# Performance work log

Hardware: AMD Instinct MI355X
Metric: run time of the kernel (lower is better)

Reference implementation:

```python
import jax, jax.numpy as jnp
import numpy as np

N = 50000      # num_nodes
E = 500000     # num_edges
D_IN = 128     # in_features
D_OUT = 128    # out_features
D_REL = 128    # nrela_dim
NEG_SLOPE = 0.2   # LeakyReLU alpha
RATIO = 0.5       # float ratio -> simple (non-schedule) branch
LN_EPS = 1e-5


def setup_inputs() -> dict:
    key = jax.random.key(0)
    ks = jax.random.split(key, 8)
    edge_index = jax.random.randint(ks[0], (2, E), 0, N, dtype=jnp.int64)
    x = jax.random.normal(ks[1], (N, D_IN), dtype=jnp.float32)
    edge_type_embed = jax.random.normal(ks[2], (E, D_REL), dtype=jnp.float32)
    # learned params (xavier-ish scale)
    W = jax.random.normal(ks[3], (4, 2 * D_OUT + D_REL, D_OUT), dtype=jnp.float32) * 0.05
    a = jax.random.normal(ks[4], (4, D_OUT, 1), dtype=jnp.float32) * 0.05
    xw = jax.random.normal(ks[5], (D_IN, D_OUT), dtype=jnp.float32) * (1.0 / np.sqrt(D_IN))
    xb = jnp.zeros((D_OUT,), dtype=jnp.float32)
    gamma = jnp.ones((D_OUT,), dtype=jnp.float32)
    beta = jnp.zeros((D_OUT,), dtype=jnp.float32)
    return {"edge_index": edge_index, "x": x, "edge_type_embed": edge_type_embed,
            "W": W, "a": a, "xw": xw, "xb": xb, "gamma": gamma, "beta": beta}


def _segment_softmax(score, seg, num_segments):
    # per-source-node softmax over edges (matches torch_geometric softmax util)
    seg_max = jax.ops.segment_max(score, seg, num_segments=num_segments)
    seg_max = jnp.where(jnp.isfinite(seg_max), seg_max, 0.0)  # empty segments
    e = jnp.exp(score - seg_max[seg])
    denom = jax.ops.segment_sum(e, seg, num_segments=num_segments)
    return e / (denom[seg] + 1e-16)


def _one_iter(edge_index, xc, ete, Wi, ai):
    src, dst = edge_index[0], edge_index[1]
    # [E, 2*D_OUT + D_REL] @ [2*D_OUT+D_REL, D_OUT] -> [E, D_OUT]
    edge_h = jnp.concatenate([xc[src], xc[dst], ete], axis=1) @ Wi
    score = jax.nn.leaky_relu(jnp.squeeze(edge_h @ ai, -1), NEG_SLOPE)  # [E]
    alpha = _segment_softmax(score, src, N)
    k = int(E * RATIO)
    _, idx = jax.lax.top_k(alpha, k)
    mask = jnp.zeros((E,), dtype=bool).at[idx].set(True)
    alpha = jnp.where(mask, alpha, 0.0)
    # scatter-add weighted messages back to source nodes
    return jax.ops.segment_sum(alpha[:, None] * edge_h, src, num_segments=N)


def reference(edge_index, x, edge_type_embed, W, a, xw, xb, gamma, beta):
    xc = x @ xw + xb  # x_linear
    for i in range(4):  # fixed 4 aggregation iterations (float-ratio branch)
        xc = _one_iter(edge_index, xc, edge_type_embed, W[i], a[i])
    xc = jax.nn.elu(xc)  # concat=True
    mu = jnp.mean(xc, axis=-1, keepdims=True)
    var = jnp.var(xc, axis=-1, keepdims=True)
    return (xc - mu) * jax.lax.rsqrt(var + LN_EPS) * gamma + beta
```

## Files before the change

### kernel.cpp

```cpp
#include <hip/hip_runtime.h>
#include <math.h>

#define DOUT 128

typedef unsigned short u16;
typedef __attribute__((ext_vector_type(8))) short bf16x8;
typedef __attribute__((ext_vector_type(4))) float f32x4;

static __device__ __forceinline__ f32x4 mfma16x16x32(bf16x8 a, bf16x8 b, f32x4 c) {
  return __builtin_amdgcn_mfma_f32_16x16x32_bf16(a, b, c, 0, 0, 0);
}

static __device__ __forceinline__ short bf16i(int v) {
  return (short)(__float_as_uint((float)v) >> 16);
}

static __device__ __forceinline__ float wsum64(float v) {
#pragma unroll
  for (int off = 32; off > 0; off >>= 1) v += __shfl_xor(v, off, 64);
  return v;
}
static __device__ __forceinline__ float wmax64(float v) {
#pragma unroll
  for (int off = 32; off > 0; off >>= 1) v = fmaxf(v, __shfl_xor(v, off, 64));
  return v;
}
static __device__ __forceinline__ float rsumg(float v) {
  v += __shfl_xor(v, 16, 64);
  v += __shfl_xor(v, 32, 64);
  return v;
}

static __device__ __forceinline__ void split3(float x, u16& h, u16& m, u16& l) {
  unsigned u = __float_as_uint(x);
  unsigned rh = u + 0x7FFFu + ((u >> 16) & 1u);
  h = (u16)(rh >> 16);
  float hf = __uint_as_float(rh & 0xFFFF0000u);
  float d1 = x - hf;
  unsigned v = __float_as_uint(d1);
  unsigned rm = v + 0x7FFFu + ((v >> 16) & 1u);
  m = (u16)(rm >> 16);
  float mf = __uint_as_float(rm & 0xFFFF0000u);
  float d2 = d1 - mf;
  unsigned w2 = __float_as_uint(d2);
  unsigned rl = w2 + 0x7FFFu + ((w2 >> 16) & 1u);
  l = (u16)(rl >> 16);
}

static __device__ __forceinline__ void split3pk(float x0, float x1,
                                                unsigned& h, unsigned& m, unsigned& l) {
  unsigned hp, mp, lp;
  asm("v_cvt_pk_bf16_f32 %0, %1, %2" : "=v"(hp) : "v"(x0), "v"(x1));
  float d0 = x0 - __uint_as_float(hp << 16);
  float d1 = x1 - __uint_as_float(hp & 0xFFFF0000u);
  asm("v_cvt_pk_bf16_f32 %0, %1, %2" : "=v"(mp) : "v"(d0), "v"(d1));
  float e0 = d0 - __uint_as_float(mp << 16);
  float e1 = d1 - __uint_as_float(mp & 0xFFFF0000u);
  asm("v_cvt_pk_bf16_f32 %0, %1, %2" : "=v"(lp) : "v"(e0), "v"(e1));
  h = hp; m = mp; l = lp;
}
static __device__ __forceinline__ void split34pk(float4 v, uint2& h, uint2& m, uint2& lo) {
  split3pk(v.x, v.y, h.x, m.x, lo.x);
  split3pk(v.z, v.w, h.y, m.y, lo.y);
}

__global__ void zero_detect_kernel(int* __restrict__ degcur, unsigned* __restrict__ hists,
                                   unsigned* __restrict__ rep, int* __restrict__ candcnt4,
                                   int N, const void* __restrict__ ei, int* __restrict__ flag,
                                   int E) {
  int i = blockIdx.x * blockDim.x + threadIdx.x;
  if (i < N) degcur[i] = 0;
  if (i < 4096) hists[i] = 0u;
  if (i < 32768) rep[i] = 0u;
  if (i < 4) candcnt4[i] = 0;
  const int* p = (const int*)ei;
  int lim = (E < 65536) ? E : 65536;
  int any = 0;
  for (int j = i; j < lim; j += gridDim.x * blockDim.x) any |= (p[2 * j + 1] != 0);
  if (__any(any))
    if ((threadIdx.x & 63) == 0 && any) atomicOr(flag, 1);
}

__global__ void cvt_deg_kernel(const void* __restrict__ ei, const int* __restrict__ flag,
                               int* __restrict__ src, int* __restrict__ dst,
                               int* __restrict__ degcur, int E) {
  int i = blockIdx.x * blockDim.x + threadIdx.x;
  if (i >= E) return;
  int s, d;
  if (*flag) { const int* p = (const int*)ei; s = p[i]; d = p[E + i]; }
  else { const long long* p = (const long long*)ei; s = (int)p[i]; d = (int)p[(size_t)E + i]; }
  src[i] = s;
  dst[i] = d;
  atomicAdd(&degcur[s], 1);
}

__global__ void scan_rowptr_kernel(int* __restrict__ degcur, int* __restrict__ rowptr, int N) {
  const int tid = threadIdx.x;
  const int lane = tid & 63, wid = tid >> 6;
  __shared__ int wsumS[16];
  __shared__ int sbase;
  if (tid == 0) sbase = 0;
  __syncthreads();
  for (int base = 0; base < N; base += 1024) {
    int i = base + tid;
    int v = (i < N) ? degcur[i] : 0;
    int x = v;
#pragma unroll
    for (int off = 1; off < 64; off <<= 1) {
      int y = __shfl_up(x, off, 64);
      if (lane >= off) x += y;
    }
    if (lane == 63) wsumS[wid] = x;
    __syncthreads();
    int wbase = 0;
#pragma unroll
    for (int w2 = 0; w2 < 16; ++w2) wbase += (w2 < wid) ? wsumS[w2] : 0;
    int excl = sbase + wbase + x - v;
    if (i < N) { rowptr[i] = excl; degcur[i] = excl; }
    __syncthreads();
    if (tid == 1023) sbase += wbase + x;
    __syncthreads();
  }
  if (tid == 0) rowptr[N] = sbase;
}

__global__ void scatter_kernel(const int* __restrict__ src, int* __restrict__ cursor,
                               int* __restrict__ eids, int E) {
  int e = blockIdx.x * blockDim.x + threadIdx.x;
  if (e >= E) return;
  int p = atomicAdd(&cursor[src[e]], 1);
  eids[p] = e;
}

__global__ void sort_eids_kernel(const int* __restrict__ rowptr, int* __restrict__ eids, int N) {
  int n = blockIdx.x * blockDim.x + threadIdx.x;
  if (n >= N) return;
  int p0 = rowptr[n], p1 = rowptr[n + 1];
  for (int i = p0 + 1; i < p1; ++i) {
    int key = eids[i];
    int j = i - 1;
    while (j >= p0 && eids[j] > key) { eids[j + 1] = eids[j]; --j; }
    eids[j + 1] = key;
  }
}

__global__ void wprep_kernel(const float* __restrict__ W, const float* __restrict__ a,
                             float* __restrict__ wa_all, const float* __restrict__ xw,
                             u16* __restrict__ wtH, u16* __restrict__ wtM,
                             u16* __restrict__ wtL) {
  int blk = blockIdx.x;
  int tid = threadIdx.x;
  if (blk < 4) {
    int it = blk, k = tid;
    const float* row = W + ((size_t)it * 384 + k) * DOUT;
    const float* ai = a + (size_t)it * DOUT;
    float acc = 0.f;
    for (int j = 0; j < DOUT; ++j) acc = fmaf(row[j], ai[j], acc);
    wa_all[it * 384 + k] = acc;
    return;
  }
  __shared__ int muS[32];
  {
    int lw = tid & 63, g = lw >> 4;
    bf16x8 aEnc;
#pragma unroll
    for (int j = 0; j < 8; ++j) aEnc[j] = bf16i(8 * g + j + 1);
    f32x4 z = {0.f, 0.f, 0.f, 0.f};
    for (int t0 = 0; t0 < 32; ++t0) {
      int g0 = t0 >> 3, j0 = t0 & 7;
      bf16x8 bOne;
#pragma unroll
      for (int j = 0; j < 8; ++j)
        bOne[j] = (g == g0 && j == j0) ? (short)0x3F80 : (short)0;
      f32x4 d = mfma16x16x32(aEnc, bOne, z);
      if (tid == t0) muS[t0] = ((int)(d[0] + 0.5f) - 1) & 31;
    }
  }
  __syncthreads();
  int b = blk - 4;
  int set, ks;
  const float* srcp;
  if (b < 4) { set = 0; ks = b; srcp = xw; }
  else { set = 1 + (b - 4) / 12; ks = (b - 4) % 12; srcp = W + (size_t)(set - 1) * 384 * DOUT; }
  size_t base = ((size_t)set * 12 + ks) * 4096;
  for (int i = tid; i < 4096; i += blockDim.x) {
    int col = i >> 5, t = i & 31;
    float x = srcp[(size_t)(ks * 32 + muS[t]) * DOUT + col];
    u16 h, m, l;
    split3(x, h, m, l);
    wtH[base + i] = h;
    wtM[base + i] = m;
    wtL[base + i] = l;
  }
}

__global__ __launch_bounds__(256) void et4_kernel(const float* __restrict__ ete,
                                                  const float* __restrict__ wa_all,
                                                  float* __restrict__ et4, int E) {
  __shared__ float4 w3s[4][32];
  int tid = threadIdx.x;
  if (tid < 128) {
    int it = tid >> 5, k4 = tid & 31;
    const float* base = wa_all + it * 384 + 256 + k4 * 4;
    w3s[it][k4] = make_float4(base[0], base[1], base[2], base[3]);
  }
  __syncthreads();
  int e = blockIdx.x * blockDim.x + tid;
  if (e >= E) return;
  const float4* row = (const float4*)(ete + (size_t)e * DOUT);
  float a0 = 0.f, a1 = 0.f, a2 = 0.f, a3 = 0.f;
#pragma unroll
  for (int k4 = 0; k4 < 32; ++k4) {
    float4 r = row[k4];
    float4 w0 = w3s[0][k4], w1 = w3s[1][k4], w2 = w3s[2][k4], w3v = w3s[3][k4];
    a0 = fmaf(r.x, w0.x, fmaf(r.y, w0.y, fmaf(r.z, w0.z, fmaf(r.w, w0.w, a0))));
    a1 = fmaf(r.x, w1.x, fmaf(r.y, w1.y, fmaf(r.z, w1.z, fmaf(r.w, w1.w, a1))));
    a2 = fmaf(r.x, w2.x, fmaf(r.y, w2.y, fmaf(r.z, w2.z, fmaf(r.w, w2.w, a2))));
    a3 = fmaf(r.x, w3v.x, fmaf(r.y, w3v.y, fmaf(r.z, w3v.z, fmaf(r.w, w3v.w, a3))));
  }
  et4[e] = a0;
  et4[(size_t)E + e] = a1;
  et4[(size_t)2 * E + e] = a2;
  et4[(size_t)3 * E + e] = a3;
}

__global__ __launch_bounds__(256) void softmax_kernel(
    const int* __restrict__ rowptr, const int* __restrict__ eids, const int* __restrict__ dst,
    const float* __restrict__ pa, const float* __restrict__ qa, const float* __restrict__ et4,
    int it, int E, float* __restrict__ alpha, unsigned* __restrict__ rep0, int N) {
  __shared__ unsigned lh[256];
  int tid = threadIdx.x;
  lh[tid] = 0u;
  __syncthreads();
  const float* etp = et4 + (size_t)it * E;
  int w = (int)(((size_t)blockIdx.x * blockDim.x + tid) >> 6);
  int lane = tid & 63;
  if (w < N) {
    int p0 = rowptr[w], p1 = rowptr[w + 1];
    int deg = p1 - p0;
    if (deg > 0) {
      float pan = pa[w];
      if (deg <= 64) {
        int p = p0 + lane;
        int e = -1;
        float sv = -3.402823466e38f;
        if (p < p1) {
          e = eids[p];
          float s = pan + qa[dst[e]] + etp[e];
          sv = (s >= 0.f) ? s : 0.2f * s;
        }
        float m = wmax64(sv);
        float ee = (e >= 0) ? expf(sv - m) : 0.f;
        float den = 0.f;
        for (int i = 0; i < deg; ++i) den += __shfl(ee, i, 64);
        den += 1e-16f;
        if (e >= 0) {
          float av = ee / den;
          alpha[e] = av;
          atomicAdd(&lh[__float_as_uint(av) >> 24], 1u);
        }
      } else if (deg <= 256) {
        float sv[4]; int ev[4];
#pragma unroll
        for (int u = 0; u < 4; ++u) {
          int p = p0 + u * 64 + lane;
          if (p < p1) {
            int e = eids[p];
            ev[u] = e;
            float s = pan + qa[dst[e]] + etp[e];
            sv[u] = (s >= 0.f) ? s : 0.2f * s;
          } else { ev[u] = -1; sv[u] = -3.402823466e38f; }
        }
        float m = fmaxf(fmaxf(sv[0], sv[1]), fmaxf(sv[2], sv[3]));
        m = wmax64(m);
        float ssum = 0.f;
#pragma unroll
        for (int u = 0; u < 4; ++u)
          if (ev[u] >= 0) { sv[u] = expf(sv[u] - m); ssum += sv[u]; }
        ssum = wsum64(ssum);
        float den = ssum + 1e-16f;
#pragma unroll
        for (int u = 0; u < 4; ++u)
          if (ev[u] >= 0) {
            float av = sv[u] / den;
            alpha[ev[u]] = av;
            atomicAdd(&lh[__float_as_uint(av) >> 24], 1u);
          }
      } else {
        float m = -3.402823466e38f;
        for (int p = p0 + lane; p < p1; p += 64) {
          int e = eids[p];
          float s = pan + qa[dst[e]] + etp[e];
          s = (s >= 0.f) ? s : 0.2f * s;
          m = fmaxf(m, s);
        }
        m = wmax64(m);
        float ssum = 0.f;
        for (int p = p0 + lane; p < p1; p += 64) {
          int e = eids[p];
          float s = pan + qa[dst[e]] + etp[e];
          s = (s >= 0.f) ? s : 0.2f * s;
          ssum += expf(s - m);
        }
        ssum = wsum64(ssum);
        float den = ssum + 1e-16f;
        for (int p = p0 + lane; p < p1; p += 64) {
          int e = eids[p];
          float s = pan + qa[dst[e]] + etp[e];
          s = (s >= 0.f) ? s : 0.2f * s;
          float av = expf(s - m) / den;
          alpha[e] = av;
          atomicAdd(&lh[__float_as_uint(av) >> 24], 1u);
        }
      }
    }
  }
  __syncthreads();
  if (lh[tid]) atomicAdd(&rep0[(blockIdx.x & 31) * 256 + tid], lh[tid]);
}

__device__ __forceinline__ void scan256_one(const unsigned* __restrict__ hist, unsigned krem_in,
                                            unsigned* lds, unsigned* res,
                                            unsigned& bin, unsigned& krem_out) {
  int t = threadIdx.x;
  lds[t] = hist[t];
  __syncthreads();
  for (int off = 1; off < 256; off <<= 1) {
    unsigned add = (t + off < 256) ? lds[t + off] : 0u;
    __syncthreads();
    lds[t] += add;
    __syncthreads();
  }
  {
    unsigned above = (t == 255) ? 0u : lds[t + 1];
    if (lds[t] >= krem_in && above < krem_in) { res[0] = (unsigned)t; res[1] = krem_in - above; }
  }
  __syncthreads();
  bin = res[0];
  krem_out = res[1];
  __syncthreads();
}

__global__ __launch_bounds__(256) void hist1_kernel(const float* __restrict__ alpha,
                                                    const unsigned* __restrict__ rep0,
                                                    unsigned* __restrict__ hists_it,
                                                    unsigned* __restrict__ scanres,
                                                    unsigned Ktop, int E) {
  __shared__ unsigned lds[256], res2[2], lh[256];
  int t = threadIdx.x;
  unsigned v = 0u;
#pragma unroll
  for (int r = 0; r < 32; ++r) v += rep0[r * 256 + t];
  lds[t] = v;
  __syncthreads();
  for (int off = 1; off < 256; off <<= 1) {
    unsigned add = (t + off < 256) ? lds[t + off] : 0u;
    __syncthreads();
    lds[t] += add;
    __syncthreads();
  }
  {
    unsigned above = (t == 255) ? 0u : lds[t + 1];
    if (lds[t] >= Ktop && above < Ktop) { res2[0] = (unsigned)t; res2[1] = Ktop - above; }
  }
  __syncthreads();
  unsigned bin0 = res2[0];
  if (blockIdx.x == 0 && t == 0) { scanres[0] = bin0; scanres[1] = res2[1]; }
  lh[t] = 0u;
  __syncthreads();
  unsigned* myh = hists_it + 256;
  for (int e = blockIdx.x * blockDim.x + t; e < E; e += gridDim.x * blockDim.x) {
    unsigned b = __float_as_uint(alpha[e]);
    if ((b >> 24) == bin0) atomicAdd(&lh[(b >> 16) & 0xFFu], 1u);
  }
  __syncthreads();
  if (lh[t]) atomicAdd(&myh[t], lh[t]);
}

__global__ __launch_bounds__(256) void hist2_kernel(const float* __restrict__ alpha,
                                                    unsigned* __restrict__ hists_it,
                                                    unsigned* __restrict__ scanres, int E) {
  __shared__ unsigned lds[256], res2[2], lh[256];
  int t = threadIdx.x;
  unsigned pref8 = scanres[0], krem0 = scanres[1];
  unsigned bin1, krem1;
  scan256_one(hists_it + 256, krem0, lds, res2, bin1, krem1);
  unsigned pref16 = (pref8 << 8) | bin1;
  if (blockIdx.x == 0 && t == 0) { scanres[2] = pref16; scanres[3] = krem1; }
  lh[t] = 0u;
  __syncthreads();
  unsigned* myh = hists_it + 512;
  for (int e = blockIdx.x * blockDim.x + t; e < E; e += gridDim.x * blockDim.x) {
    unsigned b = __float_as_uint(alpha[e]);
    if ((b >> 16) == pref16) atomicAdd(&lh[(b >> 8) & 0xFFu], 1u);
  }
  __syncthreads();
  if (lh[t]) atomicAdd(&myh[t], lh[t]);
}

__global__ __launch_bounds__(256) void hist3c_kernel(const float* __restrict__ alpha,
                                                     unsigned* __restrict__ hists_it,
                                                     unsigned* __restrict__ scanres,
                                                     int* __restrict__ candList,
                                                     int* __restrict__ candCnt, int E) {
  __shared__ unsigned lds[256], res2[2], lh[256];
  int t = threadIdx.x;
  unsigned pref16 = scanres[2], krem1 = scanres[3];
  unsigned bin2, krem2;
  scan256_one(hists_it + 512, krem1, lds, res2, bin2, krem2);
  unsigned pref24 = (pref16 << 8) | bin2;
  if (blockIdx.x == 0 && t == 0) { scanres[4] = pref24; scanres[5] = krem2; }
  lh[t] = 0u;
  __syncthreads();
  unsigned* myh = hists_it + 768;
  for (int e = blockIdx.x * blockDim.x + t; e < E; e += gridDim.x * blockDim.x) {
    unsigned b = __float_as_uint(alpha[e]);
    if ((b >> 8) == pref24) {
      atomicAdd(&lh[b & 0xFFu], 1u);
      int p = atomicAdd(candCnt, 1);
      if (p < 4096) candList[p] = e;
    }
  }
  __syncthreads();
  if (lh[t]) atomicAdd(&myh[t], lh[t]);
}

__global__ __launch_bounds__(1024) void resolve24_kernel(
    const float* __restrict__ alpha, float* __restrict__ amask,
    const unsigned* __restrict__ hists_it, const unsigned* __restrict__ scanres,
    const int* __restrict__ candList, const int* __restrict__ candCnt,
    int* __restrict__ header, int E) {
  __shared__ unsigned lds[256], res2[2];
  int tid = threadIdx.x;
  unsigned pref24 = scanres[4], krem2 = scanres[5];
  {
    int t = tid;
    if (t < 256) lds[t] = hists_it[768 + t];
    __syncthreads();
    for (int off = 1; off < 256; off <<= 1) {
      unsigned add = 0u;
      if (t < 256 && t + off < 256) add = lds[t + off];
      __syncthreads();
      if (t < 256) lds[t] += add;
      __syncthreads();
    }
    if (t < 256) {
      unsigned above = (t == 255) ? 0u : lds[t + 1];
      if (lds[t] >= krem2 && above < krem2) { res2[0] = (unsigned)t; res2[1] = krem2 - above; }
    }
    __syncthreads();
  }
  unsigned thr = (pref24 << 8) | res2[0];
  int needT = (int)res2[1];
  __syncthreads();
  int cc = *candCnt;
  __shared__ int tiel[4096];
  __shared__ int tiec;
  if (tid == 0) tiec = 0;
  __syncthreads();
  if (cc <= 4096) {
    for (int i = tid; i < cc; i += blockDim.x) {
      int e = candList[i];
      if (__float_as_uint(alpha[e]) == thr) { int p = atomicAdd(&tiec, 1); tiel[p] = e; }
    }
    __syncthreads();
    int ce = tiec;
    int dropc = ce - needT;
    if (dropc <= 0) {
      if (tid == 0) { header[0] = 0; header[1] = (int)thr; header[2] = 0; }
      return;
    }
    if (dropc <= 64) {
      int sortN = 64;
      while (sortN < ce) sortN <<= 1;
      for (int i = tid; i < sortN; i += blockDim.x)
        if (i >= ce) tiel[i] = 0x7fffffff;
      __syncthreads();
      for (int k = 2; k <= sortN; k <<= 1) {
        for (int j = k >> 1; j > 0; j >>= 1) {
          for (int i = tid; i < sortN; i += blockDim.x) {
            int ixj = i ^ j;
            if (ixj > i) {
              int v0 = tiel[i], v1 = tiel[ixj];
              bool up = ((i & k) == 0);
              if ((v0 > v1) == up) { tiel[i] = v1; tiel[ixj] = v0; }
            }
          }
          __syncthreads();
        }
      }
      if (tid == 0) { header[0] = 0; header[1] = (int)thr; header[2] = dropc; }
      for (int i = tid; i < dropc; i += blockDim.x) header[3 + i] = tiel[needT + i];
      return;
    }
  }
  if (tid == 0) { header[0] = 1; }
  __shared__ int wtot[16];
  __shared__ int sbase;
  if (tid == 0) sbase = 0;
  __syncthreads();
  int lane = tid & 63, wid = tid >> 6;
  for (int base = 0; base < E; base += 1024) {
    int e = base + tid;
    float a = 0.f; int f = 0; unsigned b = 0u;
    if (e < E) { a = alpha[e]; b = __float_as_uint(a); f = (b == thr) ? 1 : 0; }
    int x = f;
#pragma unroll
    for (int off = 1; off < 64; off <<= 1) {
      int y = __shfl_up(x, off, 64);
      if (lane >= off) x += y;
    }
    if (lane == 63) wtot[wid] = x;
    __syncthreads();
    int wbase = 0;
#pragma unroll
    for (int w2 = 0; w2 < 16; ++w2) wbase += (w2 < wid) ? wtot[w2] : 0;
    if (e < E) {
      float outv = 0.f;
      if (b > thr) outv = a;
      else if (f && (sbase + wbase + x - f) < needT) outv = a;
      amask[e] = outv;
    }
    __syncthreads();
    if (tid == 1023) sbase += wbase + x;
    __syncthreads();
  }
}

static __device__ __forceinline__ float edge_w(const float* __restrict__ alpha,
                                               const float* __restrict__ amask,
                                               const int* __restrict__ hdr, int flg,
                                               unsigned thr, int dc, int e) {
  if (flg) return amask[e];
  float av = alpha[e];
  unsigned b = __float_as_uint(av);
  if (b > thr) return av;
  if (b == thr) {
    for (int j = 0; j < dc; ++j)
      if (hdr[3 + j] == e) return 0.f;
    return av;
  }
  return 0.f;
}

__global__ void agg_kernel(const int* __restrict__ rowptr, const int* __restrict__ eids,
                           const int* __restrict__ dst, const float* __restrict__ alpha,
                           const float* __restrict__ amask, const int* __restrict__ hdr,
                           const float* __restrict__ xc, const float* __restrict__ ete,
                           float* __restrict__ sa, float* __restrict__ vbuf,
                           float* __restrict__ tbuf, int N) {
  int w = (int)(((size_t)blockIdx.x * blockDim.x + threadIdx.x) >> 6);
  int lane = threadIdx.x & 63;
  if (w >= N) return;
  const int flg = hdr[0];
  const unsigned thr = (unsigned)hdr[1];
  const int dc = hdr[2];
  int p0 = rowptr[w], p1 = rowptr[w + 1];
  int deg = p1 - p0;
  const int half = lane >> 5;
  const int l32 = lane & 31;
  const float4* xc4 = (const float4*)xc;
  const float4* et4p = (const float4*)ete;
  float4 acc = make_float4(0.f, 0.f, 0.f, 0.f);
  float s = 0.f;
  if (deg <= 64) {
    int p = p0 + lane;
    int e = -1; float am = 0.f; int dd = 0;
    if (p < p1) { e = eids[p]; am = edge_w(alpha, amask, hdr, flg, thr, dc, e); dd = dst[e]; }
    for (int i = 0; i < deg; ++i) {
      float a = __shfl(am, i, 64);
      if (a != 0.f) {
        int ei = __shfl(e, i, 64);
        int di = __shfl(dd, i, 64);
        const float4* b = half ? (et4p + (size_t)ei * 32) : (xc4 + (size_t)di * 32);
        float4 r = b[l32];
        acc.x = fmaf(a, r.x, acc.x); acc.y = fmaf(a, r.y, acc.y);
        acc.z = fmaf(a, r.z, acc.z); acc.w = fmaf(a, r.w, acc.w);
        s += a;
      }
    }
  } else {
    for (int p = p0; p < p1; ++p) {
      int e0 = eids[p];
      float a0 = edge_w(alpha, amask, hdr, flg, thr, dc, e0);
      if (a0 != 0.f) {
        int d0 = dst[e0];
        const float4* b0 = half ? (et4p + (size_t)e0 * 32) : (xc4 + (size_t)d0 * 32);
        float4 r = b0[l32];
        acc.x = fmaf(a0, r.x, acc.x); acc.y = fmaf(a0, r.y, acc.y);
        acc.z = fmaf(a0, r.z, acc.z); acc.w = fmaf(a0, r.w, acc.w);
        s += a0;
      }
    }
  }
  if (half == 0) ((float4*)vbuf)[(size_t)w * 32 + l32] = acc;
  else           ((float4*)tbuf)[(size_t)w * 32 + l32] = acc;
  if (lane == 0) sa[w] = s;
}

__global__ __launch_bounds__(256) void gemm_mfma_kernel(
    const float* __restrict__ A0, const float* __restrict__ A1, const float* __restrict__ A2,
    const float* __restrict__ sca, const u16* __restrict__ wtH, const u16* __restrict__ wtM,
    const u16* __restrict__ wtL, const float* __restrict__ bias, float* __restrict__ C,
    int N, int nseg,
    const float* __restrict__ wa_next, float* __restrict__ pa, float* __restrict__ qa,
    const float* __restrict__ gamma, const float* __restrict__ beta,
    float* __restrict__ outp, int epi) {
  __shared__ __align__(16) char smem[61440];
  u16 (*AsH)[40] = (u16(*)[40])(smem);
  u16 (*AsM)[40] = (u16(*)[40])(smem + 10240);
  u16 (*AsL)[40] = (u16(*)[40])(smem + 20480);
  u16 (*BsH)[40] = (u16(*)[40])(smem + 30720);
  u16 (*BsM)[40] = (u16(*)[40])(smem + 40960);
  u16 (*BsL)[40] = (u16(*)[40])(smem + 51200);
  const int tid = threadIdx.x;
  const int m0 = blockIdx.x * 128;
  const int K = DOUT * nseg;
  const int w = tid >> 6, l = tid & 63;
  const int cb = l & 15, g = l >> 4;

  int rowlab[4], collab[4];
  {
    bf16x8 enc, ones;
#pragma unroll
    for (int j = 0; j < 8; ++j) { enc[j] = bf16i(cb + 1); ones[j] = (short)0x3F80; }
    f32x4 z = {0.f, 0.f, 0.f, 0.f};
    f32x4 dR = mfma16x16x32(enc, ones, z);
    f32x4 dC = mfma16x16x32(ones, enc, z);
#pragma unroll
    for (int r = 0; r < 4; ++r) {
      rowlab[r] = ((int)(dR[r] * (1.f / 32.f) + 0.5f) - 1) & 15;
      collab[r] = ((int)(dC[r] * (1.f / 32.f) + 0.5f) - 1) & 15;
    }
  }

  f32x4 acc[2][8];
#pragma unroll
  for (int i = 0; i < 2; ++i)
#pragma unroll
    for (int j = 0; j < 8; ++j) acc[i][j] = (f32x4){0.f, 0.f, 0.f, 0.f};

  const int srow = tid >> 1, shalf = tid & 1;
  const int grow_s = m0 + srow;
  float scv = 1.f;
  if (sca && grow_s < N) scv = sca[grow_s];

  auto loadA = [&](int kc, float4& v0, float4& v1, float4& v2, float4& v3) {
    const int seg = kc >> 7;
    const float* Ap = (seg == 0) ? A0 : (seg == 1) ? A1 : A2;
    v0 = make_float4(0.f, 0.f, 0.f, 0.f); v1 = v0; v2 = v0; v3 = v0;
    if (grow_s < N) {
      const float4* p = (const float4*)(Ap + (size_t)grow_s * DOUT + (kc & 127) + shalf * 16);
      v0 = p[0]; v1 = p[1]; v2 = p[2]; v3 = p[3];
      if (seg == 0 && sca) {
        v0.x *= scv; v0.y *= scv; v0.z *= scv; v0.w *= scv;
        v1.x *= scv; v1.y *= scv; v1.z *= scv; v1.w *= scv;
        v2.x *= scv; v2.y *= scv; v2.z *= scv; v2.w *= scv;
        v3.x *= scv; v3.y *= scv; v3.z *= scv; v3.w *= scv;
      }
    }
  };
  auto loadB = [&](int kc, uint4& h0, uint4& h1, uint4& m0u, uint4& m1u, uint4& l0u,
                   uint4& l1u) {
    size_t sb = (size_t)(kc >> 5) << 12;
    const uint4* gh = (const uint4*)(wtH + sb) + tid * 2;
    const uint4* gm = (const uint4*)(wtM + sb) + tid * 2;
    const uint4* gl = (const uint4*)(wtL + sb) + tid * 2;
    h0 = gh[0]; h1 = gh[1];
    m0u = gm[0]; m1u = gm[1];
    l0u = gl[0]; l1u = gl[1];
  };

  float4 av0, av1, av2, av3, nv0, nv1, nv2, nv3;
  uint4 bh0, bh1, bm0u, bm1u, bl0u, bl1u, nh0, nh1, nm0, nm1, nl0, nl1;
  loadA(0, av0, av1, av2, av3);
  loadB(0, bh0, bh1, bm0u, bm1u, bl0u, bl1u);

  const int nks = K >> 5;
  for (int ks = 0; ks < nks; ++ks) {
    const int kc = ks << 5;
    {
      uint2 h0, m0v, l0, h1, m1v, l1, h2, m2v, l2, h3, m3v, l3;
      split34pk(av0, h0, m0v, l0); split34pk(av1, h1, m1v, l1);
      split34pk(av2, h2, m2v, l2); split34pk(av3, h3, m3v, l3);
      *(uint4*)&AsH[srow][shalf * 16]     = make_uint4(h0.x, h0.y, h1.x, h1.y);
      *(uint4*)&AsH[srow][shalf * 16 + 8] = make_uint4(h2.x, h2.y, h3.x, h3.y);
      *(uint4*)&AsM[srow][shalf * 16]     = make_uint4(m0v.x, m0v.y, m1v.x, m1v.y);
      *(uint4*)&AsM[srow][shalf * 16 + 8] = make_uint4(m2v.x, m2v.y, m3v.x, m3v.y);
      *(uint4*)&AsL[srow][shalf * 16]     = make_uint4(l0.x, l0.y, l1.x, l1.y);
      *(uint4*)&AsL[srow][shalf * 16 + 8] = make_uint4(l2.x, l2.y, l3.x, l3.y);
      *(uint4*)&BsH[srow][shalf * 16]     = bh0;
      *(uint4*)&BsH[srow][shalf * 16 + 8] = bh1;
      *(uint4*)&BsM[srow][shalf * 16]     = bm0u;
      *(uint4*)&BsM[srow][shalf * 16 + 8] = bm1u;
      *(uint4*)&BsL[srow][shalf * 16]     = bl0u;
      *(uint4*)&BsL[srow][shalf * 16 + 8] = bl1u;
    }
    if (ks + 1 < nks) {
      loadA(kc + 32, nv0, nv1, nv2, nv3);
      loadB(kc + 32, nh0, nh1, nm0, nm1, nl0, nl1);
    }
    __syncthreads();
    bf16x8 aH0 = *(const bf16x8*)&AsH[w * 32 + cb][g * 8];
    bf16x8 aH1 = *(const bf16x8*)&AsH[w * 32 + 16 + cb][g * 8];
    bf16x8 aM0 = *(const bf16x8*)&AsM[w * 32 + cb][g * 8];
    bf16x8 aM1 = *(const bf16x8*)&AsM[w * 32 + 16 + cb][g * 8];
    bf16x8 aL0 = *(const bf16x8*)&AsL[w * 32 + cb][g * 8];
    bf16x8 aL1 = *(const bf16x8*)&AsL[w * 32 + 16 + cb][g * 8];
#pragma unroll
    for (int ct = 0; ct < 8; ++ct) {
      bf16x8 bH = *(const bf16x8*)&BsH[ct * 16 + cb][g * 8];
      bf16x8 bM = *(const bf16x8*)&BsM[ct * 16 + cb][g * 8];
      bf16x8 bL = *(const bf16x8*)&BsL[ct * 16 + cb][g * 8];
      acc[0][ct] = mfma16x16x32(aH0, bH, acc[0][ct]);
      acc[1][ct] = mfma16x16x32(aH1, bH, acc[1][ct]);
      acc[0][ct] = mfma16x16x32(aM0, bH, acc[0][ct]);
      acc[1][ct] = mfma16x16x32(aM1, bH, acc[1][ct]);
      acc[0][ct] = mfma16x16x32(aL0, bH, acc[0][ct]);
      acc[1][ct] = mfma16x16x32(aL1, bH, acc[1][ct]);
      acc[0][ct] = mfma16x16x32(aH0, bM, acc[0][ct]);
      acc[1][ct] = mfma16x16x32(aH1, bM, acc[1][ct]);
      acc[0][ct] = mfma16x16x32(aM0, bM, acc[0][ct]);
      acc[1][ct] = mfma16x16x32(aM1, bM, acc[1][ct]);
      acc[0][ct] = mfma16x16x32(aH0, bL, acc[0][ct]);
      acc[1][ct] = mfma16x16x32(aH1, bL, acc[1][ct]);
    }
    __syncthreads();
    av0 = nv0; av1 = nv1; av2 = nv2; av3 = nv3;
    bh0 = nh0; bh1 = nh1; bm0u = nm0; bm1u = nm1; bl0u = nl0; bl1u = nl1;
  }

  float* slab = (float*)(smem + (size_t)w * 8448);
  const int row16 = l & 15;
  const int csel = (l >> 4) * 32;
#pragma unroll
  for (int rt = 0; rt < 2; ++rt) {
#pragma unroll
    for (int ct = 0; ct < 8; ++ct)
#pragma unroll
      for (int r = 0; r < 4; ++r)
        slab[rowlab[r] * 132 + ct * 16 + collab[r]] = acc[rt][ct][r];
    __syncthreads();
    int grow = m0 + w * 32 + rt * 16 + row16;
    float v[32];
#pragma unroll
    for (int q = 0; q < 8; ++q) {
      float4 t4 = *(float4*)&slab[row16 * 132 + csel + q * 4];
      v[q * 4 + 0] = t4.x; v[q * 4 + 1] = t4.y; v[q * 4 + 2] = t4.z; v[q * 4 + 3] = t4.w;
    }
    if (bias) {
#pragma unroll
      for (int q = 0; q < 8; ++q) {
        float4 bb = *(const float4*)(bias + csel + q * 4);
        v[q * 4 + 0] += bb.x; v[q * 4 + 1] += bb.y; v[q * 4 + 2] += bb.z; v[q * 4 + 3] += bb.w;
      }
    }
    if (epi == 2) {
#pragma unroll
      for (int i = 0; i < 32; ++i) v[i] = (v[i] > 0.f) ? v[i] : expm1f(v[i]);
      float s = 0.f;
#pragma unroll
      for (int i = 0; i < 32; ++i) s += v[i];
      s = rsumg(s);
      float mu = s * (1.f / 128.f);
      float sq = 0.f;
#pragma unroll
      for (int i = 0; i < 32; ++i) { float d = v[i] - mu; sq += d * d; }
      sq = rsumg(sq);
      float rstd = rsqrtf(sq * (1.f / 128.f) + 1e-5f);
      if (grow < N) {
#pragma unroll
        for (int q = 0; q < 8; ++q) {
          float4 ga = *(const float4*)(gamma + csel + q * 4);
          float4 be = *(const float4*)(beta + csel + q * 4);
          float4 o;
          o.x = (v[q * 4 + 0] - mu) * rstd * ga.x + be.x;
          o.y = (v[q * 4 + 1] - mu) * rstd * ga.y + be.y;
          o.z = (v[q * 4 + 2] - mu) * rstd * ga.z + be.z;
          o.w = (v[q * 4 + 3] - mu) * rstd * ga.w + be.w;
          *(float4*)(outp + (size_t)grow * DOUT + csel + q * 4) = o;
        }
      }
    } else {
      if (grow < N) {
#pragma unroll
        for (int q = 0; q < 8; ++q)
          *(float4*)(C + (size_t)grow * DOUT + csel + q * 4) =
              make_float4(v[q * 4 + 0], v[q * 4 + 1], v[q * 4 + 2], v[q * 4 + 3]);
      }
      if (epi == 1) {
        float pp = 0.f, qq = 0.f;
#pragma unroll
        for (int i = 0; i < 32; ++i) {
          pp = fmaf(v[i], wa_next[csel + i], pp);
          qq = fmaf(v[i], wa_next[128 + csel + i], qq);
        }
        pp = rsumg(pp);
        qq = rsumg(qq);
        if ((l >> 4) == 0 && grow < N) { pa[grow] = pp; qa[grow] = qq; }
      }
    }
    __syncthreads();
  }
}

extern "C" void kernel_launch(void* const* d_in, const int* in_sizes, int n_in,
                              void* d_out, int out_size, void* d_ws, size_t ws_size,
                              hipStream_t stream) {
  const int E = in_sizes[0] / 2;
  const int N = in_sizes[1] / DOUT;
  const unsigned Ktop = (unsigned)(E / 2);

  const void*  ei    = d_in[0];
  const float* x     = (const float*)d_in[1];
  const float* ete   = (const float*)d_in[2];
  const float* W     = (const float*)d_in[3];
  const float* a     = (const float*)d_in[4];
  const float* xw    = (const float*)d_in[5];
  const float* xb    = (const float*)d_in[6];
  const float* gamma = (const float*)d_in[7];
  const float* beta  = (const float*)d_in[8];
  float* out = (float*)d_out;

  size_t off = 0;
  auto take = [&](size_t bytes) -> char* {
    char* p = (char*)d_ws + off;
    off += (bytes + 255) & ~(size_t)255;
    return p;
  };
  int*      src32   = (int*)take((size_t)E * 4);
  int*      dst32   = (int*)take((size_t)E * 4);
  int*      rowptr  = (int*)take(((size_t)N + 1) * 4);
  int*      degcur  = (int*)take((size_t)N * 4);
  int*      eids    = (int*)take((size_t)E * 4);
  float*    pa      = (float*)take((size_t)N * 4);
  float*    qa      = (float*)take((size_t)N * 4);
  float*    wa_all  = (float*)take(4 * 384 * 4);
  float*    alpha   = (float*)take((size_t)E * 4);
  float*    amask   = (float*)take((size_t)E * 4);
  float*    sa      = (float*)take((size_t)N * 4);
  float*    vbuf    = (float*)take((size_t)N * DOUT * 4);
  float*    tbuf    = (float*)take((size_t)N * DOUT * 4);
  float*    xcA     = (float*)take((size_t)N * DOUT * 4);
  float*    xcB     = (float*)take((size_t)N * DOUT * 4);
  float*    et4     = (float*)take((size_t)E * 4 * 4);
  unsigned* hists   = (unsigned*)take(4 * 4 * 256 * 4);
  unsigned* rep     = (unsigned*)take(4 * 32 * 256 * 4);
  int*      candcnt4= (int*)take(64);
  int*      flag    = (int*)take(64);
  int*      candList= (int*)take(4096 * 4);
  int*      header  = (int*)take(4 * 80 * 4);
  u16*      wtH     = (u16*)take((size_t)5 * 12 * 4096 * 2);
  u16*      wtM     = (u16*)take((size_t)5 * 12 * 4096 * 2);
  u16*      wtL     = (u16*)take((size_t)5 * 12 * 4096 * 2);
  unsigned* scanres = (unsigned*)take(4 * 8 * 4);
  (void)ws_size; (void)n_in; (void)out_size;

  const int TB  = 256;
  const int gE  = (E + TB - 1) / TB;
  const int gN  = (N + TB - 1) / TB;
  const int gN4 = (N + 3) / 4;
  const int gM  = (N + 127) / 128;

  (void)hipMemsetAsync(flag, 0, 4, stream);
  zero_detect_kernel<<<gN, TB, 0, stream>>>(degcur, hists, rep, candcnt4, N, ei, flag, E);
  cvt_deg_kernel<<<gE, TB, 0, stream>>>(ei, flag, src32, dst32, degcur, E);
  scan_rowptr_kernel<<<1, 1024, 0, stream>>>(degcur, rowptr, N);
  scatter_kernel<<<gE, TB, 0, stream>>>(src32, degcur, eids, E);
  sort_eids_kernel<<<gN, TB, 0, stream>>>(rowptr, eids, N);
  wprep_kernel<<<56, 384, 0, stream>>>(W, a, wa_all, xw, wtH, wtM, wtL);
  et4_kernel<<<gE, TB, 0, stream>>>(ete, wa_all, et4, E);
  gemm_mfma_kernel<<<gM, 256, 0, stream>>>(x, nullptr, nullptr, nullptr, wtH, wtM, wtL, xb,
                                           xcA, N, 1, wa_all, pa, qa, nullptr, nullptr,
                                           nullptr, 1);

  float* bufs[2] = {xcA, xcB};
  for (int it = 0; it < 4; ++it) {
    const float* xc = bufs[it & 1];
    float* xn = bufs[(it & 1) ^ 1];
    unsigned* hists_it = hists + it * 1024;
    unsigned* rep_it = rep + it * 8192;
    unsigned* sres_it = scanres + it * 8;
    int* hdr_it = header + it * 80;
    const u16* wH = wtH + (size_t)(it + 1) * 12 * 4096;
    const u16* wM = wtM + (size_t)(it + 1) * 12 * 4096;
    const u16* wL = wtL + (size_t)(it + 1) * 12 * 4096;

    softmax_kernel<<<gN4, TB, 0, stream>>>(rowptr, eids, dst32, pa, qa, et4, it, E, alpha,
                                           rep_it, N);
    hist1_kernel<<<384, 256, 0, stream>>>(alpha, rep_it, hists_it, sres_it, Ktop, E);
    hist2_kernel<<<384, 256, 0, stream>>>(alpha, hists_it, sres_it, E);
    hist3c_kernel<<<384, 256, 0, stream>>>(alpha, hists_it, sres_it, candList,
                                           candcnt4 + it, E);
    resolve24_kernel<<<1, 1024, 0, stream>>>(alpha, amask, hists_it, sres_it, candList,
                                             candcnt4 + it, hdr_it, E);
    agg_kernel<<<gN4, TB, 0, stream>>>(rowptr, eids, dst32, alpha, amask, hdr_it,
                                       xc, ete, sa, vbuf, tbuf, N);
    if (it < 3)
      gemm_mfma_kernel<<<gM, 256, 0, stream>>>(xc, vbuf, tbuf, sa, wH, wM, wL, nullptr, xn,
                                               N, 3, wa_all + (it + 1) * 384, pa, qa,
                                               nullptr, nullptr, nullptr, 1);
    else
      gemm_mfma_kernel<<<gM, 256, 0, stream>>>(xc, vbuf, tbuf, sa, wH, wM, wL, nullptr, xn,
                                               N, 3, nullptr, pa, qa, gamma, beta, out, 2);
  }
}
```

Before: 853.5 us.

## Store per-edge scores and alphas in CSR order to remove indirect gathers

Edge-indexed arrays (et4 scores, alpha, destination ids) are now kept in CSR position order rather than original edge order. A permuted dst array and an inverse position map are built once in the et4 kernel. Softmax and aggregation can then read these arrays contiguously instead of going through eids and dst indirections. The tie-resolution path maps back through eids and pos to keep the original-edge-order tie-breaking. This adds two E-sized buffers and a scattered pos write, and the full masking pass now does a gathered read through pos.

New measurement: 825.3 us, median of 2. 1.03x faster.

```diff
diff --git a/kernel.cpp b/kernel.cpp
--- a/kernel.cpp
+++ b/kernel.cpp
@@ -196,6 +196,9 @@
 
 __global__ __launch_bounds__(256) void et4_kernel(const float* __restrict__ ete,
                                                   const float* __restrict__ wa_all,
+                                                  const int* __restrict__ eids,
+                                                  const int* __restrict__ dst,
+                                                  int* __restrict__ dstp, int* __restrict__ pos,
                                                   float* __restrict__ et4, int E) {
   __shared__ float4 w3s[4][32];
   int tid = threadIdx.x;
@@ -205,8 +208,11 @@
     w3s[it][k4] = make_float4(base[0], base[1], base[2], base[3]);
   }
   __syncthreads();
-  int e = blockIdx.x * blockDim.x + tid;
-  if (e >= E) return;
+  int p = blockIdx.x * blockDim.x + tid;
+  if (p >= E) return;
+  int e = eids[p];
+  dstp[p] = dst[e];
+  pos[e] = p;
   const float4* row = (const float4*)(ete + (size_t)e * DOUT);
   float a0 = 0.f, a1 = 0.f, a2 = 0.f, a3 = 0.f;
 #pragma unroll
@@ -218,14 +224,14 @@
     a2 = fmaf(r.x, w2.x, fmaf(r.y, w2.y, fmaf(r.z, w2.z, fmaf(r.w, w2.w, a2))));
     a3 = fmaf(r.x, w3v.x, fmaf(r.y, w3v.y, fmaf(r.z, w3v.z, fmaf(r.w, w3v.w, a3))));
   }
-  et4[e] = a0;
-  et4[(size_t)E + e] = a1;
-  et4[(size_t)2 * E + e] = a2;
-  et4[(size_t)3 * E + e] = a3;
+  et4[p] = a0;
+  et4[(size_t)E + p] = a1;
+  et4[(size_t)2 * E + p] = a2;
+  et4[(size_t)3 * E + p] = a3;
 }
 
 __global__ __launch_bounds__(256) void softmax_kernel(
-    const int* __restrict__ rowptr, const int* __restrict__ eids, const int* __restrict__ dst,
+    const int* __restrict__ rowptr, const int* __restrict__ dstp,
     const float* __restrict__ pa, const float* __restrict__ qa, const float* __restrict__ et4,
     int it, int E, float* __restrict__ alpha, unsigned* __restrict__ rep0, int N) {
   __shared__ unsigned lh[256];
@@ -242,74 +248,69 @@
       float pan = pa[w];
       if (deg <= 64) {
         int p = p0 + lane;
-        int e = -1;
+        int ok = (p < p1);
         float sv = -3.402823466e38f;
-        if (p < p1) {
-          e = eids[p];
-          float s = pan + qa[dst[e]] + etp[e];
+        if (ok) {
+          float s = pan + qa[dstp[p]] + etp[p];
           sv = (s >= 0.f) ? s : 0.2f * s;
         }
         float m = wmax64(sv);
-        float ee = (e >= 0) ? expf(sv - m) : 0.f;
+        float ee = ok ? expf(sv - m) : 0.f;
         float den = 0.f;
         for (int i = 0; i < deg; ++i) den += __shfl(ee, i, 64);
         den += 1e-16f;
-        if (e >= 0) {
+        if (ok) {
           float av = ee / den;
-          alpha[e] = av;
+          alpha[p] = av;
           atomicAdd(&lh[__float_as_uint(av) >> 24], 1u);
         }
       } else if (deg <= 256) {
-        float sv[4]; int ev[4];
+        float sv[4]; int okv[4];
 #pragma unroll
         for (int u = 0; u < 4; ++u) {
           int p = p0 + u * 64 + lane;
           if (p < p1) {
-            int e = eids[p];
-            ev[u] = e;
-            float s = pan + qa[dst[e]] + etp[e];
+            okv[u] = 1;
+            float s = pan + qa[dstp[p]] + etp[p];
             sv[u] = (s >= 0.f) ? s : 0.2f * s;
-          } else { ev[u] = -1; sv[u] = -3.402823466e38f; }
+          } else { okv[u] = 0; sv[u] = -3.402823466e38f; }
         }
         float m = fmaxf(fmaxf(sv[0], sv[1]), fmaxf(sv[2], sv[3]));
         m = wmax64(m);
         float ssum = 0.f;
 #pragma unroll
         for (int u = 0; u < 4; ++u)
-          if (ev[u] >= 0) { sv[u] = expf(sv[u] - m); ssum += sv[u]; }
+          if (okv[u]) { sv[u] = expf(sv[u] - m); ssum += sv[u]; }
         ssum = wsum64(ssum);
         float den = ssum + 1e-16f;
 #pragma unroll
         for (int u = 0; u < 4; ++u)
-          if (ev[u] >= 0) {
+          if (okv[u]) {
             float av = sv[u] / den;
-            alpha[ev[u]] = av;
+            alpha[p0 + u * 64 + lane] = av;
             atomicAdd(&lh[__float_as_uint(av) >> 24], 1u);
           }
       } else {
         float m = -3.402823466e38f;
         for (int p = p0 + lane; p < p1; p += 64) {
-          int e = eids[p];
-          float s = pan + qa[dst[e]] + etp[e];
+          float s = pan + qa[dstp[p]] + etp[p];
           s = (s >= 0.f) ? s : 0.2f * s;
           m = fmaxf(m, s);
         }
         m = wmax64(m);
         float ssum = 0.f;
         for (int p = p0 + lane; p < p1; p += 64) {
-          int e = eids[p];
-          float s = pan + qa[dst[e]] + etp[e];
+          float s = pan + qa[dstp[p]] + etp[p];
           s = (s >= 0.f) ? s : 0.2f * s;
           ssum += expf(s - m);
         }
         ssum = wsum64(ssum);
         float den = ssum + 1e-16f;
         for (int p = p0 + lane; p < p1; p += 64) {
-          int e = eids[p];
-          float s = pan + qa[dst[e]] + etp[e];
+          float s = pan + qa[dstp[p]] + etp[p];
           s = (s >= 0.f) ? s : 0.2f * s;
           float av = expf(s - m) / den;
-          alpha[e] = av;
+          alpha[p] = av;
           atomicAdd(&lh[__float_as_uint(av) >> 24], 1u);
         }
       }
@@ -429,6 +430,7 @@
     const float* __restrict__ alpha, float* __restrict__ amask,
     const unsigned* __restrict__ hists_it, const unsigned* __restrict__ scanres,
     const int* __restrict__ candList, const int* __restrict__ candCnt,
+    const int* __restrict__ eids, const int* __restrict__ pos,
     int* __restrict__ header, int E) {
   __shared__ unsigned lds[256], res2[2];
   int tid = threadIdx.x;
@@ -460,8 +462,11 @@
   __syncthreads();
   if (cc <= 4096) {
     for (int i = tid; i < cc; i += blockDim.x) {
-      int e = candList[i];
-      if (__float_as_uint(alpha[e]) == thr) { int p = atomicAdd(&tiec, 1); tiel[p] = e; }
+      int p = candList[i];
+      if (__float_as_uint(alpha[p]) == thr) {
+        int q = atomicAdd(&tiec, 1);
+        tiel[q] = eids[p];
+      }
     }
     __syncthreads();
     int ce = tiec;
@@ -503,7 +508,7 @@
   for (int base = 0; base < E; base += 1024) {
     int e = base + tid;
     float a = 0.f; int f = 0; unsigned b = 0u;
-    if (e < E) { a = alpha[e]; b = __float_as_uint(a); f = (b == thr) ? 1 : 0; }
+    if (e < E) { a = alpha[pos[e]]; b = __float_as_uint(a); f = (b == thr) ? 1 : 0; }
     int x = f;
 #pragma unroll
     for (int off = 1; off < 64; off <<= 1) {
@@ -527,12 +532,10 @@
   }
 }
 
-static __device__ __forceinline__ float edge_w(const float* __restrict__ alpha,
-                                               const float* __restrict__ amask,
-                                               const int* __restrict__ hdr, int flg,
-                                               unsigned thr, int dc, int e) {
+static __device__ __forceinline__ float edge_w2(float av, const float* __restrict__ amask,
+                                                const int* __restrict__ hdr, int flg,
+                                                unsigned thr, int dc, int e) {
   if (flg) return amask[e];
-  float av = alpha[e];
   unsigned b = __float_as_uint(av);
   if (b > thr) return av;
   if (b == thr) {
@@ -544,7 +547,7 @@
 }
 
 __global__ void agg_kernel(const int* __restrict__ rowptr, const int* __restrict__ eids,
-                           const int* __restrict__ dst, const float* __restrict__ alpha,
+                           const int* __restrict__ dstp, const float* __restrict__ alpha,
                            const float* __restrict__ amask, const int* __restrict__ hdr,
                            const float* __restrict__ xc, const float* __restrict__ ete,
                            float* __restrict__ sa, float* __restrict__ vbuf,
@@ -566,7 +569,7 @@
   if (deg <= 64) {
     int p = p0 + lane;
     int e = -1; float am = 0.f; int dd = 0;
-    if (p < p1) { e = eids[p]; am = edge_w(alpha, amask, hdr, flg, thr, dc, e); dd = dst[e]; }
+    if (p < p1) { e = eids[p]; am = edge_w2(alpha[p], amask, hdr, flg, thr, dc, e); dd = dstp[p]; }
     for (int i = 0; i < deg; ++i) {
       float a = __shfl(am, i, 64);
       if (a != 0.f) {
@@ -582,9 +585,9 @@
   } else {
     for (int p = p0; p < p1; ++p) {
       int e0 = eids[p];
-      float a0 = edge_w(alpha, amask, hdr, flg, thr, dc, e0);
+      float a0 = edge_w2(alpha[p], amask, hdr, flg, thr, dc, e0);
       if (a0 != 0.f) {
-        int d0 = dst[e0];
+        int d0 = dstp[p];
         const float4* b0 = half ? (et4p + (size_t)e0 * 32) : (xc4 + (size_t)d0 * 32);
         float4 r = b0[l32];
         acc.x = fmaf(a0, r.x, acc.x); acc.y = fmaf(a0, r.y, acc.y);
@@ -833,6 +836,8 @@
   int*      rowptr  = (int*)take(((size_t)N + 1) * 4);
   int*      degcur  = (int*)take((size_t)N * 4);
   int*      eids    = (int*)take((size_t)E * 4);
+  int*      dstp    = (int*)take((size_t)E * 4);
+  int*      pos     = (int*)take((size_t)E * 4);
   float*    pa      = (float*)take((size_t)N * 4);
   float*    qa      = (float*)take((size_t)N * 4);
   float*    wa_all  = (float*)take(4 * 384 * 4);
@@ -869,7 +874,7 @@
   scatter_kernel<<<gE, TB, 0, stream>>>(src32, degcur, eids, E);
   sort_eids_kernel<<<gN, TB, 0, stream>>>(rowptr, eids, N);
   wprep_kernel<<<56, 384, 0, stream>>>(W, a, wa_all, xw, wtH, wtM, wtL);
-  et4_kernel<<<gE, TB, 0, stream>>>(ete, wa_all, et4, E);
+  et4_kernel<<<gE, TB, 0, stream>>>(ete, wa_all, eids, dst32, dstp, pos, et4, E);
   gemm_mfma_kernel<<<gM, 256, 0, stream>>>(x, nullptr, nullptr, nullptr, wtH, wtM, wtL, xb,
                                            xcA, N, 1, wa_all, pa, qa, nullptr, nullptr,
                                            nullptr, 1);
@@ -886,15 +891,15 @@
     const u16* wM = wtM + (size_t)(it + 1) * 12 * 4096;
     const u16* wL = wtL + (size_t)(it + 1) * 12 * 4096;
 
-    softmax_kernel<<<gN4, TB, 0, stream>>>(rowptr, eids, dst32, pa, qa, et4, it, E, alpha,
+    softmax_kernel<<<gN4, TB, 0, stream>>>(rowptr, dstp, pa, qa, et4, it, E, alpha,
                                            rep_it, N);
     hist1_kernel<<<384, 256, 0, stream>>>(alpha, rep_it, hists_it, sres_it, Ktop, E);
     hist2_kernel<<<384, 256, 0, stream>>>(alpha, hists_it, sres_it, E);
     hist3c_kernel<<<384, 256, 0, stream>>>(alpha, hists_it, sres_it, candList,
                                            candcnt4 + it, E);
     resolve24_kernel<<<1, 1024, 0, stream>>>(alpha, amask, hists_it, sres_it, candList,
-                                             candcnt4 + it, hdr_it, E);
-    agg_kernel<<<gN4, TB, 0, stream>>>(rowptr, eids, dst32, alpha, amask, hdr_it,
+                                             candcnt4 + it, eids, pos, hdr_it, E);
+    agg_kernel<<<gN4, TB, 0, stream>>>(rowptr, eids, dstp, alpha, amask, hdr_it,
                                        xc, ete, sa, vbuf, tbuf, N);
     if (it < 3)
       gemm_mfma_kernel<<<gM, 256, 0, stream>>>(xc, vbuf, tbuf, sa, wH, wM, wL, nullptr, xn,
```
